# Kernel optimization log

Measured on AMD Instinct MI355X. Metric: run time of the kernel, lower is better.

## Reference

```python
import jax, jax.numpy as jnp
import numpy as np

N, C, S = 16, 512, 4096

def setup_inputs() -> dict:
    rng = jax.random.key(0)
    k1, k2, k3 = jax.random.split(rng, 3)
    return {
        "key": jax.random.normal(k1, (N, C, S), dtype=jnp.float32),
        "value": jax.random.normal(k2, (N, C, S), dtype=jnp.float32),
        "query": jax.random.normal(k3, (N, C, S), dtype=jnp.float32),
    }

def reference(key, value, query):
    KC = key.shape[1]
    # query.permute(0,2,1): [N, C, S] -> [N, S, C]
    # sim_map = bmm(key, query^T): [N, C, C], scaled by KC^-0.5
    sim = jnp.einsum("ncs,nds->ncd", key, query) * (KC ** -0.5)
    # softmax over dim=1 (first C axis)
    sim = jax.nn.softmax(sim, axis=1)
    # context = bmm(sim, value): [N, C, C] @ [N, C, S] -> [N, C, S]
    context = jnp.einsum("ncd,nds->ncs", sim, value)
    return context
```

## Files before the change

### kernel.cpp

```cpp
#include <hip/hip_runtime.h>

typedef __bf16 bf16x8 __attribute__((ext_vector_type(8)));
typedef float f32x4 __attribute__((ext_vector_type(4)));
typedef unsigned short u16;
typedef u16 u16x4 __attribute__((ext_vector_type(4)));
typedef u16 u16x8 __attribute__((ext_vector_type(8)));

__device__ __forceinline__ u16 f2bf(float f) {
  unsigned u = __builtin_bit_cast(unsigned, f);
  unsigned r = (u + 0x7fffu + ((u >> 16) & 1u)) >> 16;
  return (u16)r;
}

__device__ __forceinline__ void gld_lds16(const u16* g, u16* l) {
  __builtin_amdgcn_global_load_lds(
      (__attribute__((address_space(1))) void*)(g),
      (__attribute__((address_space(3))) void*)(l), 16, 0, 0);
}

__device__ __forceinline__ f32x4 ntload4(const float* p) {
  return __builtin_nontemporal_load((const f32x4*)p);
}

__global__ __launch_bounds__(256) void k_cvt(const float* __restrict__ K,
                                             const float* __restrict__ Q,
                                             u16* __restrict__ Kb,
                                             u16* __restrict__ Qb) {
  const float* src = blockIdx.y ? Q : K;
  u16* dst = blockIdx.y ? Qb : Kb;
  const size_t base = (size_t)blockIdx.x * 4096;
  const int t = threadIdx.x;
  f32x4 v[4];
#pragma unroll
  for (int c = 0; c < 4; ++c)
    v[c] = ntload4(src + base + c * 1024 + t * 4);
#pragma unroll
  for (int c = 0; c < 4; ++c) {
    u16x4 h;
    h[0] = f2bf(v[c][0]); h[1] = f2bf(v[c][1]); h[2] = f2bf(v[c][2]); h[3] = f2bf(v[c][3]);
    *(u16x4*)(dst + base + c * 1024 + t * 4) = h;
  }
}

template <int KDIV>
__global__ __launch_bounds__(512) void k_simk(const u16* __restrict__ Kb,
                                              const u16* __restrict__ Qb,
                                              float* __restrict__ Lp) {
  __shared__ u16 sA[2][128 * 64];
  __shared__ u16 sB[2][128 * 64];
  constexpr int NB = 256 * KDIV;
  const int bid = blockIdx.x;
  const int sid = (bid & 7) * (NB / 8) + (bid >> 3);
  constexpr int PER_N = 16 * KDIV;
  const int n = sid / PER_N;
  const int rem = sid % PER_N;
  const int kc = rem >> 4;
  const int r2 = rem & 15;
  const int cy = r2 >> 2, dx = r2 & 3;
  const int t = threadIdx.x, lane = t & 63, wid = t >> 6;
  const int wr = wid >> 2, wc = wid & 3;
  const float scale = 0.04419417382415922f;

  const u16* Ab = Kb + ((size_t)n * 512 + cy * 128) * 4096 + kc * (4096 / KDIV);
  const u16* Bb = Qb + ((size_t)n * 512 + dx * 128) * 4096 + kc * (4096 / KDIV);
  f32x4 acc[4][2] = {};
  const int srow0 = t >> 3;
  const int scol = ((t & 7) << 3) ^ ((srow0 & 7) << 3);

#define SIM_STAGE(buf, k0)                                                      \
  {                                                                             \
    _Pragma("unroll") for (int q = 0; q < 2; ++q) {                             \
      const int row = q * 64 + srow0;                                           \
      gld_lds16(Ab + (size_t)row * 4096 + (k0) + scol,                          \
                &sA[buf][(q * 512 + (wid << 6)) * 8]);                          \
      gld_lds16(Bb + (size_t)row * 4096 + (k0) + scol,                          \
                &sB[buf][(q * 512 + (wid << 6)) * 8]);                          \
    }                                                                           \
  }
#define SIM_COMPUTE(buf)                                                        \
  {                                                                             \
    _Pragma("unroll") for (int ki = 0; ki < 2; ++ki) {                          \
      bf16x8 a[4], b[2];                                                        \
      const int ce = ki * 32 + (lane >> 4) * 8;                                 \
      _Pragma("unroll") for (int mi = 0; mi < 4; ++mi) {                        \
        const int r = wr * 64 + mi * 16 + (lane & 15);                          \
        a[mi] = *(const bf16x8*)&sA[buf][r * 64 + (ce ^ ((r & 7) << 3))];       \
      }                                                                         \
      _Pragma("unroll") for (int ni = 0; ni < 2; ++ni) {                        \
        const int r = wc * 32 + ni * 16 + (lane & 15);                          \
        b[ni] = *(const bf16x8*)&sB[buf][r * 64 + (ce ^ ((r & 7) << 3))];       \
      }                                                                         \
      _Pragma("unroll") for (int mi = 0; mi < 4; ++mi)                          \
        _Pragma("unroll") for (int ni = 0; ni < 2; ++ni)                        \
          acc[mi][ni] = __builtin_amdgcn_mfma_f32_16x16x32_bf16(                \
              a[mi], b[ni], acc[mi][ni], 0, 0, 0);                              \
    }                                                                           \
  }

  constexpr int NSTEP = 64 / KDIV;
  SIM_STAGE(0, 0);
  __syncthreads();
  int cur = 0;
  for (int kt = 0; kt < NSTEP - 1; ++kt) {
    SIM_STAGE(cur ^ 1, (kt + 1) << 6);
    SIM_COMPUTE(cur);
    __syncthreads();
    cur ^= 1;
  }
  SIM_COMPUTE(cur);

  float* Lb = Lp + ((size_t)kc * 16 + n) * 512 * 512;
  const int c0 = cy * 128, d0 = dx * 128;
#pragma unroll
  for (int mi = 0; mi < 4; ++mi)
#pragma unroll
    for (int ni = 0; ni < 2; ++ni) {
      int colo = d0 + wc * 32 + ni * 16 + (lane & 15);
#pragma unroll
      for (int j = 0; j < 4; ++j) {
        int rowo = c0 + wr * 64 + mi * 16 + ((lane >> 4) << 2) + j;
        Lb[(size_t)rowo * 512 + colo] = acc[mi][ni][j] * scale;
      }
    }
#undef SIM_STAGE
#undef SIM_COMPUTE
}

__global__ __launch_bounds__(512) void k_mix(const u16* __restrict__ Kb,
                                             const u16* __restrict__ Qb,
                                             float* __restrict__ Lp,
                                             const float* __restrict__ V,
                                             u16* __restrict__ Vt) {
  extern __shared__ char raw[];
  const int bid = blockIdx.x;
  const int t = threadIdx.x;

  if (bid % 5 == 0) {
    u16* sA = (u16*)raw;
    u16* sB = (u16*)(raw + 32768);
    const int sid0 = bid / 5;
    const int sid = (sid0 & 7) * 64 + (sid0 >> 3);
    const int n = sid >> 5;
    const int rem = sid & 31;
    const int kc = rem >> 4;
    const int r2 = rem & 15;
    const int cy = r2 >> 2, dx = r2 & 3;
    const int lane = t & 63, wid = t >> 6;
    const int wr = wid >> 2, wc = wid & 3;
    const float scale = 0.04419417382415922f;

    const u16* Ab = Kb + ((size_t)n * 512 + cy * 128) * 4096 + kc * 2048;
    const u16* Bb = Qb + ((size_t)n * 512 + dx * 128) * 4096 + kc * 2048;
    f32x4 acc[4][2] = {};
    const int srow0 = t >> 3;
    const int scol = ((t & 7) << 3) ^ ((srow0 & 7) << 3);

#define MIX_STAGE(buf, k0)                                                      \
  {                                                                             \
    _Pragma("unroll") for (int q = 0; q < 2; ++q) {                             \
      const int row = q * 64 + srow0;                                           \
      gld_lds16(Ab + (size_t)row * 4096 + (k0) + scol,                          \
                sA + (buf) * 8192 + (q * 512 + (wid << 6)) * 8);                \
      gld_lds16(Bb + (size_t)row * 4096 + (k0) + scol,                          \
                sB + (buf) * 8192 + (q * 512 + (wid << 6)) * 8);                \
    }                                                                           \
  }
#define MIX_COMPUTE(buf)                                                        \
  {                                                                             \
    _Pragma("unroll") for (int ki = 0; ki < 2; ++ki) {                          \
      bf16x8 a[4], b[2];                                                        \
      const int ce = ki * 32 + (lane >> 4) * 8;                                 \
      _Pragma("unroll") for (int mi = 0; mi < 4; ++mi) {                        \
        const int r = wr * 64 + mi * 16 + (lane & 15);                          \
        a[mi] = *(const bf16x8*)&sA[(buf) * 8192 + r * 64 + (ce ^ ((r & 7) << 3))]; \
      }                                                                         \
      _Pragma("unroll") for (int ni = 0; ni < 2; ++ni) {                        \
        const int r = wc * 32 + ni * 16 + (lane & 15);                          \
        b[ni] = *(const bf16x8*)&sB[(buf) * 8192 + r * 64 + (ce ^ ((r & 7) << 3))]; \
      }                                                                         \
      _Pragma("unroll") for (int mi = 0; mi < 4; ++mi)                          \
        _Pragma("unroll") for (int ni = 0; ni < 2; ++ni)                        \
          acc[mi][ni] = __builtin_amdgcn_mfma_f32_16x16x32_bf16(                \
              a[mi], b[ni], acc[mi][ni], 0, 0, 0);                              \
    }                                                                           \
  }

    MIX_STAGE(0, 0);
    __syncthreads();
    int cur = 0;
    for (int kt = 0; kt < 31; ++kt) {
      MIX_STAGE(cur ^ 1, (kt + 1) << 6);
      MIX_COMPUTE(cur);
      __syncthreads();
      cur ^= 1;
    }
    MIX_COMPUTE(cur);

    float* Lb = Lp + ((size_t)kc * 16 + n) * 512 * 512;
    const int c0 = cy * 128, d0 = dx * 128;
#pragma unroll
    for (int mi = 0; mi < 4; ++mi)
#pragma unroll
      for (int ni = 0; ni < 2; ++ni) {
        int colo = d0 + wc * 32 + ni * 16 + (lane & 15);
#pragma unroll
        for (int j = 0; j < 4; ++j) {
          int rowo = c0 + wr * 64 + mi * 16 + ((lane >> 4) << 2) + j;
          Lb[(size_t)rowo * 512 + colo] = acc[mi][ni][j] * scale;
        }
      }
#undef MIX_STAGE
#undef MIX_COMPUTE
  } else {
    const int vid = bid - bid / 5 - 1;
    const int sub = t >> 8, tt = t & 255;
    const int tile = vid * 2 + sub;
    const int n = tile >> 8;
    const int r = tile & 255;
    const int d0 = (r >> 6) * 128, s0 = (r & 63) * 64;
    float* lds = (float*)(raw + sub * 34816);
    {
      const int r0 = tt >> 4, c4 = (tt & 15) << 2;
#pragma unroll
      for (int p = 0; p < 8; ++p) {
        const int dr = r0 + p * 16;
        f32x4 v = ntload4(V + ((size_t)n * 512 + d0 + dr) * 4096 + s0 + c4);
        const int sw = ((dr >> 3) & 7) << 2;
        *(f32x4*)(&lds[dr * 68 + (c4 ^ sw)]) = v;
      }
    }
    __syncthreads();
    {
      const int sr0 = tt >> 4, dcol = (tt & 15) << 3;
#pragma unroll
      for (int p2 = 0; p2 < 4; ++p2) {
        const int sr = sr0 + p2 * 16;
        u16x8 h;
#pragma unroll
        for (int j = 0; j < 8; ++j) {
          const int d = dcol + j;
          h[j] = f2bf(lds[d * 68 + (sr ^ (((d >> 3) & 7) << 2))]);
        }
        *(u16x8*)(Vt + ((size_t)n * 4096 + s0 + sr) * 512 + d0 + dcol) = h;
      }
    }
  }
}

template <int KDIV>
__global__ __launch_bounds__(256) void k_stats(const float* __restrict__ Lp,
                                               u16* __restrict__ E) {
  __shared__ float redm[8][32];
  __shared__ float reds[8][32];
  const int n = blockIdx.y;
  const int d0 = blockIdx.x * 32;
  const int tx = threadIdx.x & 31, ty = threadIdx.x >> 5;
  const size_t CH = (size_t)16 * 512 * 512;
  const float* B = Lp + (size_t)n * 512 * 512 + d0 + tx;

  float m = -3.0e38f, s = 0.f;
  for (int c = ty; c < 512; c += 8) {
    float v = B[(size_t)c * 512];
#pragma unroll
    for (int q = 1; q < KDIV; ++q) v += B[q * CH + (size_t)c * 512];
    float nm = fmaxf(m, v);
    s = s * __expf(m - nm) + __expf(v - nm);
    m = nm;
  }
  redm[ty][tx] = m;
  reds[ty][tx] = s;
  __syncthreads();
  float M = redm[0][tx];
#pragma unroll
  for (int q = 1; q < 8; ++q) M = fmaxf(M, redm[q][tx]);
  float S = 0.f;
#pragma unroll
  for (int q = 0; q < 8; ++q) S += reds[q][tx] * __expf(redm[q][tx] - M);
  const float si = 1.0f / S;

  u16* Eb = E + (size_t)n * 512 * 512 + d0 + tx;
  for (int c = ty; c < 512; c += 8) {
    float v = B[(size_t)c * 512];
#pragma unroll
    for (int q = 1; q < KDIV; ++q) v += B[q * CH + (size_t)c * 512];
    Eb[(size_t)c * 512] = f2bf(__expf(v - M) * si);
  }
}

__global__ __launch_bounds__(256) void k_vt(const float* __restrict__ V,
                                            u16* __restrict__ Vt) {
  __shared__ float lds[128 * 68];
  const int n = blockIdx.z, d0 = blockIdx.y * 128, s0 = blockIdx.x * 64;
  const int t = threadIdx.x;
  {
    const int r0 = t >> 4, c4 = (t & 15) << 2;
#pragma unroll
    for (int p = 0; p < 8; ++p) {
      const int dr = r0 + p * 16;
      f32x4 v = ntload4(V + ((size_t)n * 512 + d0 + dr) * 4096 + s0 + c4);
      const int sw = ((dr >> 3) & 7) << 2;
      *(f32x4*)(&lds[dr * 68 + (c4 ^ sw)]) = v;
    }
  }
  __syncthreads();
  {
    const int sr0 = t >> 4, dcol = (t & 15) << 3;
#pragma unroll
    for (int p2 = 0; p2 < 4; ++p2) {
      const int sr = sr0 + p2 * 16;
      u16x8 h;
#pragma unroll
      for (int j = 0; j < 8; ++j) {
        const int d = dcol + j;
        h[j] = f2bf(lds[d * 68 + (sr ^ (((d >> 3) & 7) << 2))]);
      }
      *(u16x8*)(Vt + ((size_t)n * 4096 + s0 + sr) * 512 + d0 + dcol) = h;
    }
  }
}

__global__ __launch_bounds__(256) void k_ctx2(const u16* __restrict__ E,
                                              const u16* __restrict__ Vt,
                                              float* __restrict__ O) {
  __shared__ u16 sA[128 * 64];
  __shared__ u16 sB[128 * 64];
  const int bid = blockIdx.x;
  const int sid = (bid & 7) * 256 + (bid >> 3);
  const int n = sid >> 7;
  const int rem = sid & 127;
  const int cy = rem >> 5, sx = rem & 31;
  const int t = threadIdx.x, lane = t & 63, wid = t >> 6;
  const int wr = wid >> 1, wc = wid & 1;

  const u16* Ab = E + ((size_t)n * 512 + cy * 128) * 512;
  const u16* Bb = Vt + ((size_t)n * 4096 + sx * 128) * 512;
  const int srow0 = t >> 3;
  const int scol = ((t & 7) << 3) ^ ((srow0 & 7) << 3);
  f32x4 acc[4][4] = {};

  for (int kd = 0; kd < 512; kd += 64) {
#pragma unroll
    for (int p = 0; p < 4; ++p) {
      const int row = srow0 + p * 32;
      gld_lds16(Ab + (size_t)row * 512 + kd + scol, &sA[(p * 256 + (wid << 6)) * 8]);
      gld_lds16(Bb + (size_t)row * 512 + kd + scol, &sB[(p * 256 + (wid << 6)) * 8]);
    }
    __syncthreads();
#pragma unroll
    for (int ki = 0; ki < 2; ++ki) {
      bf16x8 a[4], b[4];
      const int ce = ki * 32 + (lane >> 4) * 8;
#pragma unroll
      for (int mi = 0; mi < 4; ++mi) {
        const int r = wr * 64 + mi * 16 + (lane & 15);
        a[mi] = *(const bf16x8*)&sA[r * 64 + (ce ^ ((r & 7) << 3))];
      }
#pragma unroll
      for (int ni = 0; ni < 4; ++ni) {
        const int r = wc * 64 + ni * 16 + (lane & 15);
        b[ni] = *(const bf16x8*)&sB[r * 64 + (ce ^ ((r & 7) << 3))];
      }
#pragma unroll
      for (int mi = 0; mi < 4; ++mi)
#pragma unroll
        for (int ni = 0; ni < 4; ++ni)
          acc[mi][ni] = __builtin_amdgcn_mfma_f32_16x16x32_bf16(a[mi], b[ni], acc[mi][ni], 0, 0, 0);
    }
    __syncthreads();
  }
  float* Ob = O + ((size_t)n * 512 + cy * 128) * 4096 + sx * 128;
#pragma unroll
  for (int mi = 0; mi < 4; ++mi)
#pragma unroll
    for (int ni = 0; ni < 4; ++ni) {
      int colo = wc * 64 + ni * 16 + (lane & 15);
#pragma unroll
      for (int j = 0; j < 4; ++j) {
        int rowo = wr * 64 + mi * 16 + ((lane >> 4) << 2) + j;
        __builtin_nontemporal_store(acc[mi][ni][j], &Ob[(size_t)rowo * 4096 + colo]);
      }
    }
}

extern "C" void kernel_launch(void* const* d_in, const int* in_sizes, int n_in,
                              void* d_out, int out_size, void* d_ws, size_t ws_size,
                              hipStream_t stream) {
  const float* Kp = (const float*)d_in[0];
  const float* Vp = (const float*)d_in[1];
  const float* Qp = (const float*)d_in[2];
  float* Op = (float*)d_out;
  char* ws = (char*)d_ws;
  const size_t MB = 1024 * 1024;

  if (ws_size >= 192 * MB) {
    u16* Kb = (u16*)ws;
    u16* Qb = (u16*)(ws + 64 * MB);
    u16* Vt = (u16*)(ws + 128 * MB);
    u16* E  = (u16*)(ws + 64 * MB);
    float* Lp = Op;

    k_cvt<<<dim3(8192, 2), 256, 0, stream>>>(Kp, Qp, Kb, Qb);
    k_mix<<<2560, 512, 69632, stream>>>(Kb, Qb, Lp, Vp, Vt);
    k_stats<2><<<dim3(16, 16), 256, 0, stream>>>(Lp, E);
    k_ctx2<<<2048, 256, 0, stream>>>(E, Vt, Op);
  } else if (ws_size >= 128 * MB) {
    u16* Kb = (u16*)ws;
    u16* Qb = (u16*)(ws + 64 * MB);
    u16* Vt = (u16*)ws;
    u16* E  = (u16*)(ws + 64 * MB);
    float* Lp = Op;

    k_cvt<<<dim3(8192, 2), 256, 0, stream>>>(Kp, Qp, Kb, Qb);
    k_simk<2><<<512, 512, 0, stream>>>(Kb, Qb, Lp);
    k_stats<2><<<dim3(16, 16), 256, 0, stream>>>(Lp, E);
    k_vt<<<dim3(64, 4, 16), 256, 0, stream>>>(Vp, Vt);
    k_ctx2<<<2048, 256, 0, stream>>>(E, Vt, Op);
  }
}
```

Measured before the change: 241.8 us.

## Fuse K/Q bf16 conversion into similarity GEMM by loading fp32 tiles directly

```diff
diff --git a/kernel.cpp b/kernel.cpp
--- a/kernel.cpp
+++ b/kernel.cpp
@@ -12,6 +12,18 @@
   return (u16)r;
 }
 
+__device__ __forceinline__ bf16x8 cvt8v(f32x4 a, f32x4 b) {
+  bf16x8 h;
+  h[0] = (__bf16)a[0]; h[1] = (__bf16)a[1]; h[2] = (__bf16)a[2]; h[3] = (__bf16)a[3];
+  h[4] = (__bf16)b[0]; h[5] = (__bf16)b[1]; h[6] = (__bf16)b[2]; h[7] = (__bf16)b[3];
+  return h;
+}
+
+__device__ __forceinline__ void gld_lds16f(const float* g, float* l) {
+  __builtin_amdgcn_global_load_lds(
+      (__attribute__((address_space(1))) void*)(g),
+      (__attribute__((address_space(3))) void*)(l), 16, 0, 0);
+}
 __device__ __forceinline__ void gld_lds16(const u16* g, u16* l) {
   __builtin_amdgcn_global_load_lds(
       (__attribute__((address_space(1))) void*)(g),
@@ -20,6 +32,205 @@
 
 __device__ __forceinline__ f32x4 ntload4(const float* p) {
   return __builtin_nontemporal_load((const f32x4*)p);
+}
+
+__global__ __launch_bounds__(512) void k_mixf(const float* __restrict__ K,
+                                              const float* __restrict__ Q,
+                                              float* __restrict__ Lp,
+                                              const float* __restrict__ V,
+                                              u16* __restrict__ Vt) {
+  extern __shared__ char raw[];
+  const int bid = blockIdx.x;
+  const int t = threadIdx.x;
+
+  if (bid % 5 == 0) {
+    float* sAf = (float*)raw;
+    float* sBf = (float*)(raw + 32768);
+    const int sid0 = bid / 5;
+    const int sid = (sid0 & 7) * 64 + (sid0 >> 3);
+    const int n = sid >> 5;
+    const int rem = sid & 31;
+    const int kc = rem >> 4;
+    const int r2 = rem & 15;
+    const int cy = r2 >> 2, dx = r2 & 3;
+    const int lane = t & 63, wid = t >> 6;
+    const int wr = wid >> 2, wc = wid & 3;
+    const float scale = 0.04419417382415922f;
+
+    const float* Ab = K + ((size_t)n * 512 + cy * 128) * 4096 + kc * 2048;
+    const float* Bb = Q + ((size_t)n * 512 + dx * 128) * 4096 + kc * 2048;
+    f32x4 acc[4][2] = {};
+
+    const int srow0 = t >> 3;
+    const int scol = ((t & 7) << 2) ^ ((srow0 & 7) << 2);
+
+#define MF_STAGE(buf, k0)                                                       \
+  {                                                                             \
+    _Pragma("unroll") for (int q = 0; q < 2; ++q) {                             \
+      const int row = q * 64 + srow0;                                           \
+      gld_lds16f(Ab + (size_t)row * 4096 + (k0) + scol,                         \
+                 sAf + (buf) * 4096 + (q * 512 + (wid << 6)) * 4);              \
+      gld_lds16f(Bb + (size_t)row * 4096 + (k0) + scol,                         \
+                 sBf + (buf) * 4096 + (q * 512 + (wid << 6)) * 4);              \
+    }                                                                           \
+  }
+#define MF_COMPUTE(buf)                                                         \
+  {                                                                             \
+    bf16x8 a[4], b[2];                                                          \
+    const int cb = (lane >> 4) << 3;                                            \
+    _Pragma("unroll") for (int mi = 0; mi < 4; ++mi) {                          \
+      const int r = wr * 64 + mi * 16 + (lane & 15);                            \
+      const int sz = (r & 7) << 2;                                              \
+      const float* p = sAf + (buf) * 4096 + r * 32;                             \
+      a[mi] = cvt8v(*(const f32x4*)(p + (cb ^ sz)),                             \
+                    *(const f32x4*)(p + ((cb + 4) ^ sz)));                      \
+    }                                                                           \
+    _Pragma("unroll") for (int ni = 0; ni < 2; ++ni) {                          \
+      const int r = wc * 32 + ni * 16 + (lane & 15);                            \
+      const int sz = (r & 7) << 2;                                              \
+      const float* p = sBf + (buf) * 4096 + r * 32;                             \
+      b[ni] = cvt8v(*(const f32x4*)(p + (cb ^ sz)),                             \
+                    *(const f32x4*)(p + ((cb + 4) ^ sz)));                      \
+    }                                                                           \
+    _Pragma("unroll") for (int mi = 0; mi < 4; ++mi)                            \
+      _Pragma("unroll") for (int ni = 0; ni < 2; ++ni)                          \
+        acc[mi][ni] = __builtin_amdgcn_mfma_f32_16x16x32_bf16(                  \
+            a[mi], b[ni], acc[mi][ni], 0, 0, 0);                                \
+  }
+
+    MF_STAGE(0, 0);
+    __syncthreads();
+    int cur = 0;
+#pragma unroll 1
+    for (int kt = 0; kt < 63; ++kt) {
+      MF_STAGE(cur ^ 1, (kt + 1) * 32);
+      MF_COMPUTE(cur);
+      __syncthreads();
+      cur ^= 1;
+    }
+    MF_COMPUTE(cur);
+
+    float* Lb = Lp + ((size_t)kc * 16 + n) * 512 * 512;
+    const int c0 = cy * 128, d0 = dx * 128;
+#pragma unroll
+    for (int mi = 0; mi < 4; ++mi)
+#pragma unroll
+      for (int ni = 0; ni < 2; ++ni) {
+        int colo = d0 + wc * 32 + ni * 16 + (lane & 15);
+#pragma unroll
+        for (int j = 0; j < 4; ++j) {
+          int rowo = c0 + wr * 64 + mi * 16 + ((lane >> 4) << 2) + j;
+          Lb[(size_t)rowo * 512 + colo] = acc[mi][ni][j] * scale;
+        }
+      }
+#undef MF_STAGE
+#undef MF_COMPUTE
+  } else {
+    const int vid = bid - bid / 5 - 1;
+    const int sub = t >> 8, tt = t & 255;
+    const int tile = vid * 2 + sub;
+    const int n = tile >> 8;
+    const int r = tile & 255;
+    const int d0 = (r >> 6) * 128, s0 = (r & 63) * 64;
+    float* lds = (float*)(raw + sub * 34816);
+    {
+      const int r0 = tt >> 4, c4 = (tt & 15) << 2;
+#pragma unroll
+      for (int p = 0; p < 8; ++p) {
+        const int dr = r0 + p * 16;
+        f32x4 v = ntload4(V + ((size_t)n * 512 + d0 + dr) * 4096 + s0 + c4);
+        const int sw = ((dr >> 3) & 7) << 2;
+        *(f32x4*)(&lds[dr * 68 + (c4 ^ sw)]) = v;
+      }
+    }
+    __syncthreads();
+    {
+      const int sr0 = tt >> 4, dcol = (tt & 15) << 3;
+#pragma unroll
+      for (int p2 = 0; p2 < 4; ++p2) {
+        const int sr = sr0 + p2 * 16;
+        u16x8 h;
+#pragma unroll
+        for (int j = 0; j < 8; ++j) {
+          const int d = dcol + j;
+          h[j] = f2bf(lds[d * 68 + (sr ^ (((d >> 3) & 7) << 2))]);
+        }
+        *(u16x8*)(Vt + ((size_t)n * 4096 + s0 + sr) * 512 + d0 + dcol) = h;
+      }
+    }
+  }
+}
+
+template <int KDIV>
+__global__ __launch_bounds__(256) void k_stats(const float* __restrict__ Lp,
+                                               u16* __restrict__ E) {
+  __shared__ float redm[8][32];
+  __shared__ float reds[8][32];
+  const int n = blockIdx.y;
+  const int d0 = blockIdx.x * 32;
+  const int tx = threadIdx.x & 31, ty = threadIdx.x >> 5;
+  const size_t CH = (size_t)16 * 512 * 512;
+  const float* B = Lp + (size_t)n * 512 * 512 + d0 + tx;
+
+  float m = -3.0e38f, s = 0.f;
+  for (int c = ty; c < 512; c += 8) {
+    float v = B[(size_t)c * 512];
+#pragma unroll
+    for (int q = 1; q < KDIV; ++q) v += B[q * CH + (size_t)c * 512];
+    float nm = fmaxf(m, v);
+    s = s * __expf(m - nm) + __expf(v - nm);
+    m = nm;
+  }
+  redm[ty][tx] = m;
+  reds[ty][tx] = s;
+  __syncthreads();
+  float M = redm[0][tx];
+#pragma unroll
+  for (int q = 1; q < 8; ++q) M = fmaxf(M, redm[q][tx]);
+  float S = 0.f;
+#pragma unroll
+  for (int q = 0; q < 8; ++q) S += reds[q][tx] * __expf(redm[q][tx] - M);
+  const float si = 1.0f / S;
+
+  u16* Eb = E + (size_t)n * 512 * 512 + d0 + tx;
+  for (int c = ty; c < 512; c += 8) {
+    float v = B[(size_t)c * 512];
+#pragma unroll
+    for (int q = 1; q < KDIV; ++q) v += B[q * CH + (size_t)c * 512];
+    Eb[(size_t)c * 512] = f2bf(__expf(v - M) * si);
+  }
+}
+
+__global__ __launch_bounds__(256) void k_vt(const float* __restrict__ V,
+                                            u16* __restrict__ Vt) {
+  __shared__ float lds[128 * 68];
+  const int n = blockIdx.z, d0 = blockIdx.y * 128, s0 = blockIdx.x * 64;
+  const int t = threadIdx.x;
+  {
+    const int r0 = t >> 4, c4 = (t & 15) << 2;
+#pragma unroll
+    for (int p = 0; p < 8; ++p) {
+      const int dr = r0 + p * 16;
+      f32x4 v = ntload4(V + ((size_t)n * 512 + d0 + dr) * 4096 + s0 + c4);
+      const int sw = ((dr >> 3) & 7) << 2;
+      *(f32x4*)(&lds[dr * 68 + (c4 ^ sw)]) = v;
+    }
+  }
+  __syncthreads();
+  {
+    const int sr0 = t >> 4, dcol = (t & 15) << 3;
+#pragma unroll
+    for (int p2 = 0; p2 < 4; ++p2) {
+      const int sr = sr0 + p2 * 16;
+      u16x8 h;
+#pragma unroll
+      for (int j = 0; j < 8; ++j) {
+        const int d = dcol + j;
+        h[j] = f2bf(lds[d * 68 + (sr ^ (((d >> 3) & 7) << 2))]);
+      }
+      *(u16x8*)(Vt + ((size_t)n * 4096 + s0 + sr) * 512 + d0 + dcol) = h;
+    }
+  }
 }
 
 __global__ __launch_bounds__(256) void k_cvt(const float* __restrict__ K,
@@ -126,199 +337,6 @@
 #undef SIM_COMPUTE
 }
 
-__global__ __launch_bounds__(512) void k_mix(const u16* __restrict__ Kb,
-                                             const u16* __restrict__ Qb,
-                                             float* __restrict__ Lp,
-                                             const float* __restrict__ V,
-                                             u16* __restrict__ Vt) {
-  extern __shared__ char raw[];
-  const int bid = blockIdx.x;
-  const int t = threadIdx.x;
-
-  if (bid % 5 == 0) {
-    u16* sA = (u16*)raw;
-    u16* sB = (u16*)(raw + 32768);
-    const int sid0 = bid / 5;
-    const int sid = (sid0 & 7) * 64 + (sid0 >> 3);
-    const int n = sid >> 5;
-    const int rem = sid & 31;
-    const int kc = rem >> 4;
-    const int r2 = rem & 15;
-    const int cy = r2 >> 2, dx = r2 & 3;
-    const int lane = t & 63, wid = t >> 6;
-    const int wr = wid >> 2, wc = wid & 3;
-    const float scale = 0.04419417382415922f;
-
-    const u16* Ab = Kb + ((size_t)n * 512 + cy * 128) * 4096 + kc * 2048;
-    const u16* Bb = Qb + ((size_t)n * 512 + dx * 128) * 4096 + kc * 2048;
-    f32x4 acc[4][2] = {};
-    const int srow0 = t >> 3;
-    const int scol = ((t & 7) << 3) ^ ((srow0 & 7) << 3);
-
-#define MIX_STAGE(buf, k0)                                                      \
-  {                                                                             \
-    _Pragma("unroll") for (int q = 0; q < 2; ++q) {                             \
-      const int row = q * 64 + srow0;                                           \
-      gld_lds16(Ab + (size_t)row * 4096 + (k0) + scol,                          \
-                sA + (buf) * 8192 + (q * 512 + (wid << 6)) * 8);                \
-      gld_lds16(Bb + (size_t)row * 4096 + (k0) + scol,                          \
-                sB + (buf) * 8192 + (q * 512 + (wid << 6)) * 8);                \
-    }                                                                           \
-  }
-#define MIX_COMPUTE(buf)                                                        \
-  {                                                                             \
-    _Pragma("unroll") for (int ki = 0; ki < 2; ++ki) {                          \
-      bf16x8 a[4], b[2];                                                        \
-      const int ce = ki * 32 + (lane >> 4) * 8;                                 \
-      _Pragma("unroll") for (int mi = 0; mi < 4; ++mi) {                        \
-        const int r = wr * 64 + mi * 16 + (lane & 15);                          \
-        a[mi] = *(const bf16x8*)&sA[(buf) * 8192 + r * 64 + (ce ^ ((r & 7) << 3))]; \
-      }                                                                         \
-      _Pragma("unroll") for (int ni = 0; ni < 2; ++ni) {                        \
-        const int r = wc * 32 + ni * 16 + (lane & 15);                          \
-        b[ni] = *(const bf16x8*)&sB[(buf) * 8192 + r * 64 + (ce ^ ((r & 7) << 3))]; \
-      }                                                                         \
-      _Pragma("unroll") for (int mi = 0; mi < 4; ++mi)                          \
-        _Pragma("unroll") for (int ni = 0; ni < 2; ++ni)                        \
-          acc[mi][ni] = __builtin_amdgcn_mfma_f32_16x16x32_bf16(                \
-              a[mi], b[ni], acc[mi][ni], 0, 0, 0);                              \
-    }                                                                           \
-  }
-
-    MIX_STAGE(0, 0);
-    __syncthreads();
-    int cur = 0;
-    for (int kt = 0; kt < 31; ++kt) {
-      MIX_STAGE(cur ^ 1, (kt + 1) << 6);
-      MIX_COMPUTE(cur);
-      __syncthreads();
-      cur ^= 1;
-    }
-    MIX_COMPUTE(cur);
-
-    float* Lb = Lp + ((size_t)kc * 16 + n) * 512 * 512;
-    const int c0 = cy * 128, d0 = dx * 128;
-#pragma unroll
-    for (int mi = 0; mi < 4; ++mi)
-#pragma unroll
-      for (int ni = 0; ni < 2; ++ni) {
-        int colo = d0 + wc * 32 + ni * 16 + (lane & 15);
-#pragma unroll
-        for (int j = 0; j < 4; ++j) {
-          int rowo = c0 + wr * 64 + mi * 16 + ((lane >> 4) << 2) + j;
-          Lb[(size_t)rowo * 512 + colo] = acc[mi][ni][j] * scale;
-        }
-      }
-#undef MIX_STAGE
-#undef MIX_COMPUTE
-  } else {
-    const int vid = bid - bid / 5 - 1;
-    const int sub = t >> 8, tt = t & 255;
-    const int tile = vid * 2 + sub;
-    const int n = tile >> 8;
-    const int r = tile & 255;
-    const int d0 = (r >> 6) * 128, s0 = (r & 63) * 64;
-    float* lds = (float*)(raw + sub * 34816);
-    {
-      const int r0 = tt >> 4, c4 = (tt & 15) << 2;
-#pragma unroll
-      for (int p = 0; p < 8; ++p) {
-        const int dr = r0 + p * 16;
-        f32x4 v = ntload4(V + ((size_t)n * 512 + d0 + dr) * 4096 + s0 + c4);
-        const int sw = ((dr >> 3) & 7) << 2;
-        *(f32x4*)(&lds[dr * 68 + (c4 ^ sw)]) = v;
-      }
-    }
-    __syncthreads();
-    {
-      const int sr0 = tt >> 4, dcol = (tt & 15) << 3;
-#pragma unroll
-      for (int p2 = 0; p2 < 4; ++p2) {
-        const int sr = sr0 + p2 * 16;
-        u16x8 h;
-#pragma unroll
-        for (int j = 0; j < 8; ++j) {
-          const int d = dcol + j;
-          h[j] = f2bf(lds[d * 68 + (sr ^ (((d >> 3) & 7) << 2))]);
-        }
-        *(u16x8*)(Vt + ((size_t)n * 4096 + s0 + sr) * 512 + d0 + dcol) = h;
-      }
-    }
-  }
-}
-
-template <int KDIV>
-__global__ __launch_bounds__(256) void k_stats(const float* __restrict__ Lp,
-                                               u16* __restrict__ E) {
-  __shared__ float redm[8][32];
-  __shared__ float reds[8][32];
-  const int n = blockIdx.y;
-  const int d0 = blockIdx.x * 32;
-  const int tx = threadIdx.x & 31, ty = threadIdx.x >> 5;
-  const size_t CH = (size_t)16 * 512 * 512;
-  const float* B = Lp + (size_t)n * 512 * 512 + d0 + tx;
-
-  float m = -3.0e38f, s = 0.f;
-  for (int c = ty; c < 512; c += 8) {
-    float v = B[(size_t)c * 512];
-#pragma unroll
-    for (int q = 1; q < KDIV; ++q) v += B[q * CH + (size_t)c * 512];
-    float nm = fmaxf(m, v);
-    s = s * __expf(m - nm) + __expf(v - nm);
-    m = nm;
-  }
-  redm[ty][tx] = m;
-  reds[ty][tx] = s;
-  __syncthreads();
-  float M = redm[0][tx];
-#pragma unroll
-  for (int q = 1; q < 8; ++q) M = fmaxf(M, redm[q][tx]);
-  float S = 0.f;
-#pragma unroll
-  for (int q = 0; q < 8; ++q) S += reds[q][tx] * __expf(redm[q][tx] - M);
-  const float si = 1.0f / S;
-
-  u16* Eb = E + (size_t)n * 512 * 512 + d0 + tx;
-  for (int c = ty; c < 512; c += 8) {
-    float v = B[(size_t)c * 512];
-#pragma unroll
-    for (int q = 1; q < KDIV; ++q) v += B[q * CH + (size_t)c * 512];
-    Eb[(size_t)c * 512] = f2bf(__expf(v - M) * si);
-  }
-}
-
-__global__ __launch_bounds__(256) void k_vt(const float* __restrict__ V,
-                                            u16* __restrict__ Vt) {
-  __shared__ float lds[128 * 68];
-  const int n = blockIdx.z, d0 = blockIdx.y * 128, s0 = blockIdx.x * 64;
-  const int t = threadIdx.x;
-  {
-    const int r0 = t >> 4, c4 = (t & 15) << 2;
-#pragma unroll
-    for (int p = 0; p < 8; ++p) {
-      const int dr = r0 + p * 16;
-      f32x4 v = ntload4(V + ((size_t)n * 512 + d0 + dr) * 4096 + s0 + c4);
-      const int sw = ((dr >> 3) & 7) << 2;
-      *(f32x4*)(&lds[dr * 68 + (c4 ^ sw)]) = v;
-    }
-  }
-  __syncthreads();
-  {
-    const int sr0 = t >> 4, dcol = (t & 15) << 3;
-#pragma unroll
-    for (int p2 = 0; p2 < 4; ++p2) {
-      const int sr = sr0 + p2 * 16;
-      u16x8 h;
-#pragma unroll
-      for (int j = 0; j < 8; ++j) {
-        const int d = dcol + j;
-        h[j] = f2bf(lds[d * 68 + (sr ^ (((d >> 3) & 7) << 2))]);
-      }
-      *(u16x8*)(Vt + ((size_t)n * 4096 + s0 + sr) * 512 + d0 + dcol) = h;
-    }
-  }
-}
-
 __global__ __launch_bounds__(256) void k_ctx2(const u16* __restrict__ E,
                                               const u16* __restrict__ Vt,
                                               float* __restrict__ O) {
@@ -392,28 +410,21 @@
   char* ws = (char*)d_ws;
   const size_t MB = 1024 * 1024;
 
-  if (ws_size >= 192 * MB) {
-    u16* Kb = (u16*)ws;
-    u16* Qb = (u16*)(ws + 64 * MB);
-    u16* Vt = (u16*)(ws + 128 * MB);
-    u16* E  = (u16*)(ws + 64 * MB);
-    float* Lp = Op;
-
-    k_cvt<<<dim3(8192, 2), 256, 0, stream>>>(Kp, Qp, Kb, Qb);
-    k_mix<<<2560, 512, 69632, stream>>>(Kb, Qb, Lp, Vp, Vt);
-    k_stats<2><<<dim3(16, 16), 256, 0, stream>>>(Lp, E);
-    k_ctx2<<<2048, 256, 0, stream>>>(E, Vt, Op);
-  } else if (ws_size >= 128 * MB) {
-    u16* Kb = (u16*)ws;
-    u16* Qb = (u16*)(ws + 64 * MB);
+  if (ws_size >= 128 * MB) {
     u16* Vt = (u16*)ws;
     u16* E  = (u16*)(ws + 64 * MB);
     float* Lp = Op;
 
-    k_cvt<<<dim3(8192, 2), 256, 0, stream>>>(Kp, Qp, Kb, Qb);
-    k_simk<2><<<512, 512, 0, stream>>>(Kb, Qb, Lp);
+    k_mixf<<<2560, 512, 69632, stream>>>(Kp, Qp, Lp, Vp, Vt);
     k_stats<2><<<dim3(16, 16), 256, 0, stream>>>(Lp, E);
-    k_vt<<<dim3(64, 4, 16), 256, 0, stream>>>(Vp, Vt);
     k_ctx2<<<2048, 256, 0, stream>>>(E, Vt, Op);
-  }
-}
+  } else if (ws_size >= 72 * MB) {
+    u16* Vt = (u16*)ws;
+    u16* E  = (u16*)(ws + 64 * MB);
+    float* Lp = Op;
+
+    k_mixf<<<2560, 512, 69632, stream>>>(Kp, Qp, Lp, Vp, Vt);
+    k_stats<2><<<dim3(16, 16), 256, 0, stream>>>(Lp, E);
+    k_ctx2<<<2048, 256, 0, stream>>>(E, Vt, Op);
+  }
+}
```

Result: slower. 257.2 us (+6.3%).

## Double-buffer context GEMM with 8 waves and raise MFMA priority in sim

Applied to the files above, without the earlier changes.

```diff
diff --git a/kernel.cpp b/kernel.cpp
--- a/kernel.cpp
+++ b/kernel.cpp
@@ -39,6 +39,169 @@
     u16x4 h;
     h[0] = f2bf(v[c][0]); h[1] = f2bf(v[c][1]); h[2] = f2bf(v[c][2]); h[3] = f2bf(v[c][3]);
     *(u16x4*)(dst + base + c * 1024 + t * 4) = h;
+  }
+}
+
+__global__ __launch_bounds__(512) void k_mix(const u16* __restrict__ Kb,
+                                             const u16* __restrict__ Qb,
+                                             float* __restrict__ Lp,
+                                             const float* __restrict__ V,
+                                             u16* __restrict__ Vt) {
+  extern __shared__ char raw[];
+  const int bid = blockIdx.x;
+  const int t = threadIdx.x;
+
+  if (bid % 5 == 0) {
+    u16* sA = (u16*)raw;
+    u16* sB = (u16*)(raw + 32768);
+    const int sid0 = bid / 5;
+    const int sid = (sid0 & 7) * 64 + (sid0 >> 3);
+    const int n = sid >> 5;
+    const int rem = sid & 31;
+    const int kc = rem >> 4;
+    const int r2 = rem & 15;
+    const int cy = r2 >> 2, dx = r2 & 3;
+    const int lane = t & 63, wid = t >> 6;
+    const int wr = wid >> 2, wc = wid & 3;
+    const float scale = 0.04419417382415922f;
+
+    const u16* Ab = Kb + ((size_t)n * 512 + cy * 128) * 4096 + kc * 2048;
+    const u16* Bb = Qb + ((size_t)n * 512 + dx * 128) * 4096 + kc * 2048;
+    f32x4 acc[4][2] = {};
+    const int srow0 = t >> 3;
+    const int scol = ((t & 7) << 3) ^ ((srow0 & 7) << 3);
+
+#define MIX_STAGE(buf, k0)                                                      \
+  {                                                                             \
+    _Pragma("unroll") for (int q = 0; q < 2; ++q) {                             \
+      const int row = q * 64 + srow0;                                           \
+      gld_lds16(Ab + (size_t)row * 4096 + (k0) + scol,                          \
+                sA + (buf) * 8192 + (q * 512 + (wid << 6)) * 8);                \
+      gld_lds16(Bb + (size_t)row * 4096 + (k0) + scol,                          \
+                sB + (buf) * 8192 + (q * 512 + (wid << 6)) * 8);                \
+    }                                                                           \
+  }
+#define MIX_COMPUTE(buf)                                                        \
+  {                                                                             \
+    _Pragma("unroll") for (int ki = 0; ki < 2; ++ki) {                          \
+      bf16x8 a[4], b[2];                                                        \
+      const int ce = ki * 32 + (lane >> 4) * 8;                                 \
+      _Pragma("unroll") for (int mi = 0; mi < 4; ++mi) {                        \
+        const int r = wr * 64 + mi * 16 + (lane & 15);                          \
+        a[mi] = *(const bf16x8*)&sA[(buf) * 8192 + r * 64 + (ce ^ ((r & 7) << 3))]; \
+      }                                                                         \
+      _Pragma("unroll") for (int ni = 0; ni < 2; ++ni) {                        \
+        const int r = wc * 32 + ni * 16 + (lane & 15);                          \
+        b[ni] = *(const bf16x8*)&sB[(buf) * 8192 + r * 64 + (ce ^ ((r & 7) << 3))]; \
+      }                                                                         \
+      __builtin_amdgcn_s_setprio(1);                                            \
+      _Pragma("unroll") for (int mi = 0; mi < 4; ++mi)                          \
+        _Pragma("unroll") for (int ni = 0; ni < 2; ++ni)                        \
+          acc[mi][ni] = __builtin_amdgcn_mfma_f32_16x16x32_bf16(                \
+              a[mi], b[ni], acc[mi][ni], 0, 0, 0);                              \
+      __builtin_amdgcn_s_setprio(0);                                            \
+    }                                                                           \
+  }
+
+    MIX_STAGE(0, 0);
+    __syncthreads();
+    int cur = 0;
+    for (int kt = 0; kt < 31; ++kt) {
+      MIX_STAGE(cur ^ 1, (kt + 1) << 6);
+      MIX_COMPUTE(cur);
+      __syncthreads();
+      cur ^= 1;
+    }
+    MIX_COMPUTE(cur);
+
+    float* Lb = Lp + ((size_t)kc * 16 + n) * 512 * 512;
+    const int c0 = cy * 128, d0 = dx * 128;
+#pragma unroll
+    for (int mi = 0; mi < 4; ++mi)
+#pragma unroll
+      for (int ni = 0; ni < 2; ++ni) {
+        int colo = d0 + wc * 32 + ni * 16 + (lane & 15);
+#pragma unroll
+        for (int j = 0; j < 4; ++j) {
+          int rowo = c0 + wr * 64 + mi * 16 + ((lane >> 4) << 2) + j;
+          Lb[(size_t)rowo * 512 + colo] = acc[mi][ni][j] * scale;
+        }
+      }
+#undef MIX_STAGE
+#undef MIX_COMPUTE
+  } else {
+    const int vid = bid - bid / 5 - 1;
+    const int sub = t >> 8, tt = t & 255;
+    const int tile = vid * 2 + sub;
+    const int n = tile >> 8;
+    const int r = tile & 255;
+    const int d0 = (r >> 6) * 128, s0 = (r & 63) * 64;
+    float* lds = (float*)(raw + sub * 34816);
+    {
+      const int r0 = tt >> 4, c4 = (tt & 15) << 2;
+#pragma unroll
+      for (int p = 0; p < 8; ++p) {
+        const int dr = r0 + p * 16;
+        f32x4 v = ntload4(V + ((size_t)n * 512 + d0 + dr) * 4096 + s0 + c4);
+        const int sw = ((dr >> 3) & 7) << 2;
+        *(f32x4*)(&lds[dr * 68 + (c4 ^ sw)]) = v;
+      }
+    }
+    __syncthreads();
+    {
+      const int sr0 = tt >> 4, dcol = (tt & 15) << 3;
+#pragma unroll
+      for (int p2 = 0; p2 < 4; ++p2) {
+        const int sr = sr0 + p2 * 16;
+        u16x8 h;
+#pragma unroll
+        for (int j = 0; j < 8; ++j) {
+          const int d = dcol + j;
+          h[j] = f2bf(lds[d * 68 + (sr ^ (((d >> 3) & 7) << 2))]);
+        }
+        *(u16x8*)(Vt + ((size_t)n * 4096 + s0 + sr) * 512 + d0 + dcol) = h;
+      }
+    }
+  }
+}
+
+template <int KDIV>
+__global__ __launch_bounds__(256) void k_stats(const float* __restrict__ Lp,
+                                               u16* __restrict__ E) {
+  __shared__ float redm[8][32];
+  __shared__ float reds[8][32];
+  const int n = blockIdx.y;
+  const int d0 = blockIdx.x * 32;
+  const int tx = threadIdx.x & 31, ty = threadIdx.x >> 5;
+  const size_t CH = (size_t)16 * 512 * 512;
+  const float* B = Lp + (size_t)n * 512 * 512 + d0 + tx;
+
+  float m = -3.0e38f, s = 0.f;
+  for (int c = ty; c < 512; c += 8) {
+    float v = B[(size_t)c * 512];
+#pragma unroll
+    for (int q = 1; q < KDIV; ++q) v += B[q * CH + (size_t)c * 512];
+    float nm = fmaxf(m, v);
+    s = s * __expf(m - nm) + __expf(v - nm);
+    m = nm;
+  }
+  redm[ty][tx] = m;
+  reds[ty][tx] = s;
+  __syncthreads();
+  float M = redm[0][tx];
+#pragma unroll
+  for (int q = 1; q < 8; ++q) M = fmaxf(M, redm[q][tx]);
+  float S = 0.f;
+#pragma unroll
+  for (int q = 0; q < 8; ++q) S += reds[q][tx] * __expf(redm[q][tx] - M);
+  const float si = 1.0f / S;
+
+  u16* Eb = E + (size_t)n * 512 * 512 + d0 + tx;
+  for (int c = ty; c < 512; c += 8) {
+    float v = B[(size_t)c * 512];
+#pragma unroll
+    for (int q = 1; q < KDIV; ++q) v += B[q * CH + (size_t)c * 512];
+    Eb[(size_t)c * 512] = f2bf(__expf(v - M) * si);
   }
 }
 
@@ -126,167 +289,6 @@
 #undef SIM_COMPUTE
 }
 
-__global__ __launch_bounds__(512) void k_mix(const u16* __restrict__ Kb,
-                                             const u16* __restrict__ Qb,
-                                             float* __restrict__ Lp,
-                                             const float* __restrict__ V,
-                                             u16* __restrict__ Vt) {
-  extern __shared__ char raw[];
-  const int bid = blockIdx.x;
-  const int t = threadIdx.x;
-
-  if (bid % 5 == 0) {
-    u16* sA = (u16*)raw;
-    u16* sB = (u16*)(raw + 32768);
-    const int sid0 = bid / 5;
-    const int sid = (sid0 & 7) * 64 + (sid0 >> 3);
-    const int n = sid >> 5;
-    const int rem = sid & 31;
-    const int kc = rem >> 4;
-    const int r2 = rem & 15;
-    const int cy = r2 >> 2, dx = r2 & 3;
-    const int lane = t & 63, wid = t >> 6;
-    const int wr = wid >> 2, wc = wid & 3;
-    const float scale = 0.04419417382415922f;
-
-    const u16* Ab = Kb + ((size_t)n * 512 + cy * 128) * 4096 + kc * 2048;
-    const u16* Bb = Qb + ((size_t)n * 512 + dx * 128) * 4096 + kc * 2048;
-    f32x4 acc[4][2] = {};
-    const int srow0 = t >> 3;
-    const int scol = ((t & 7) << 3) ^ ((srow0 & 7) << 3);
-
-#define MIX_STAGE(buf, k0)                                                      \
-  {                                                                             \
-    _Pragma("unroll") for (int q = 0; q < 2; ++q) {                             \
-      const int row = q * 64 + srow0;                                           \
-      gld_lds16(Ab + (size_t)row * 4096 + (k0) + scol,                          \
-                sA + (buf) * 8192 + (q * 512 + (wid << 6)) * 8);                \
-      gld_lds16(Bb + (size_t)row * 4096 + (k0) + scol,                          \
-                sB + (buf) * 8192 + (q * 512 + (wid << 6)) * 8);                \
-    }                                                                           \
-  }
-#define MIX_COMPUTE(buf)                                                        \
-  {                                                                             \
-    _Pragma("unroll") for (int ki = 0; ki < 2; ++ki) {                          \
-      bf16x8 a[4], b[2];                                                        \
-      const int ce = ki * 32 + (lane >> 4) * 8;                                 \
-      _Pragma("unroll") for (int mi = 0; mi < 4; ++mi) {                        \
-        const int r = wr * 64 + mi * 16 + (lane & 15);                          \
-        a[mi] = *(const bf16x8*)&sA[(buf) * 8192 + r * 64 + (ce ^ ((r & 7) << 3))]; \
-      }                                                                         \
-      _Pragma("unroll") for (int ni = 0; ni < 2; ++ni) {                        \
-        const int r = wc * 32 + ni * 16 + (lane & 15);                          \
-        b[ni] = *(const bf16x8*)&sB[(buf) * 8192 + r * 64 + (ce ^ ((r & 7) << 3))]; \
-      }                                                                         \
-      _Pragma("unroll") for (int mi = 0; mi < 4; ++mi)                          \
-        _Pragma("unroll") for (int ni = 0; ni < 2; ++ni)                        \
-          acc[mi][ni] = __builtin_amdgcn_mfma_f32_16x16x32_bf16(                \
-              a[mi], b[ni], acc[mi][ni], 0, 0, 0);                              \
-    }                                                                           \
-  }
-
-    MIX_STAGE(0, 0);
-    __syncthreads();
-    int cur = 0;
-    for (int kt = 0; kt < 31; ++kt) {
-      MIX_STAGE(cur ^ 1, (kt + 1) << 6);
-      MIX_COMPUTE(cur);
-      __syncthreads();
-      cur ^= 1;
-    }
-    MIX_COMPUTE(cur);
-
-    float* Lb = Lp + ((size_t)kc * 16 + n) * 512 * 512;
-    const int c0 = cy * 128, d0 = dx * 128;
-#pragma unroll
-    for (int mi = 0; mi < 4; ++mi)
-#pragma unroll
-      for (int ni = 0; ni < 2; ++ni) {
-        int colo = d0 + wc * 32 + ni * 16 + (lane & 15);
-#pragma unroll
-        for (int j = 0; j < 4; ++j) {
-          int rowo = c0 + wr * 64 + mi * 16 + ((lane >> 4) << 2) + j;
-          Lb[(size_t)rowo * 512 + colo] = acc[mi][ni][j] * scale;
-        }
-      }
-#undef MIX_STAGE
-#undef MIX_COMPUTE
-  } else {
-    const int vid = bid - bid / 5 - 1;
-    const int sub = t >> 8, tt = t & 255;
-    const int tile = vid * 2 + sub;
-    const int n = tile >> 8;
-    const int r = tile & 255;
-    const int d0 = (r >> 6) * 128, s0 = (r & 63) * 64;
-    float* lds = (float*)(raw + sub * 34816);
-    {
-      const int r0 = tt >> 4, c4 = (tt & 15) << 2;
-#pragma unroll
-      for (int p = 0; p < 8; ++p) {
-        const int dr = r0 + p * 16;
-        f32x4 v = ntload4(V + ((size_t)n * 512 + d0 + dr) * 4096 + s0 + c4);
-        const int sw = ((dr >> 3) & 7) << 2;
-        *(f32x4*)(&lds[dr * 68 + (c4 ^ sw)]) = v;
-      }
-    }
-    __syncthreads();
-    {
-      const int sr0 = tt >> 4, dcol = (tt & 15) << 3;
-#pragma unroll
-      for (int p2 = 0; p2 < 4; ++p2) {
-        const int sr = sr0 + p2 * 16;
-        u16x8 h;
-#pragma unroll
-        for (int j = 0; j < 8; ++j) {
-          const int d = dcol + j;
-          h[j] = f2bf(lds[d * 68 + (sr ^ (((d >> 3) & 7) << 2))]);
-        }
-        *(u16x8*)(Vt + ((size_t)n * 4096 + s0 + sr) * 512 + d0 + dcol) = h;
-      }
-    }
-  }
-}
-
-template <int KDIV>
-__global__ __launch_bounds__(256) void k_stats(const float* __restrict__ Lp,
-                                               u16* __restrict__ E) {
-  __shared__ float redm[8][32];
-  __shared__ float reds[8][32];
-  const int n = blockIdx.y;
-  const int d0 = blockIdx.x * 32;
-  const int tx = threadIdx.x & 31, ty = threadIdx.x >> 5;
-  const size_t CH = (size_t)16 * 512 * 512;
-  const float* B = Lp + (size_t)n * 512 * 512 + d0 + tx;
-
-  float m = -3.0e38f, s = 0.f;
-  for (int c = ty; c < 512; c += 8) {
-    float v = B[(size_t)c * 512];
-#pragma unroll
-    for (int q = 1; q < KDIV; ++q) v += B[q * CH + (size_t)c * 512];
-    float nm = fmaxf(m, v);
-    s = s * __expf(m - nm) + __expf(v - nm);
-    m = nm;
-  }
-  redm[ty][tx] = m;
-  reds[ty][tx] = s;
-  __syncthreads();
-  float M = redm[0][tx];
-#pragma unroll
-  for (int q = 1; q < 8; ++q) M = fmaxf(M, redm[q][tx]);
-  float S = 0.f;
-#pragma unroll
-  for (int q = 0; q < 8; ++q) S += reds[q][tx] * __expf(redm[q][tx] - M);
-  const float si = 1.0f / S;
-
-  u16* Eb = E + (size_t)n * 512 * 512 + d0 + tx;
-  for (int c = ty; c < 512; c += 8) {
-    float v = B[(size_t)c * 512];
-#pragma unroll
-    for (int q = 1; q < KDIV; ++q) v += B[q * CH + (size_t)c * 512];
-    Eb[(size_t)c * 512] = f2bf(__expf(v - M) * si);
-  }
-}
-
 __global__ __launch_bounds__(256) void k_vt(const float* __restrict__ V,
                                             u16* __restrict__ Vt) {
   __shared__ float lds[128 * 68];
@@ -319,67 +321,80 @@
   }
 }
 
-__global__ __launch_bounds__(256) void k_ctx2(const u16* __restrict__ E,
+__global__ __launch_bounds__(512) void k_ctx3(const u16* __restrict__ E,
                                               const u16* __restrict__ Vt,
                                               float* __restrict__ O) {
-  __shared__ u16 sA[128 * 64];
-  __shared__ u16 sB[128 * 64];
+  __shared__ u16 sA[2][128 * 64];
+  __shared__ u16 sB[2][128 * 64];
   const int bid = blockIdx.x;
   const int sid = (bid & 7) * 256 + (bid >> 3);
   const int n = sid >> 7;
   const int rem = sid & 127;
   const int cy = rem >> 5, sx = rem & 31;
   const int t = threadIdx.x, lane = t & 63, wid = t >> 6;
-  const int wr = wid >> 1, wc = wid & 1;
+  const int wr = wid >> 2, wc = wid & 3;
 
   const u16* Ab = E + ((size_t)n * 512 + cy * 128) * 512;
   const u16* Bb = Vt + ((size_t)n * 4096 + sx * 128) * 512;
   const int srow0 = t >> 3;
   const int scol = ((t & 7) << 3) ^ ((srow0 & 7) << 3);
-  f32x4 acc[4][4] = {};
-
-  for (int kd = 0; kd < 512; kd += 64) {
-#pragma unroll
-    for (int p = 0; p < 4; ++p) {
-      const int row = srow0 + p * 32;
-      gld_lds16(Ab + (size_t)row * 512 + kd + scol, &sA[(p * 256 + (wid << 6)) * 8]);
-      gld_lds16(Bb + (size_t)row * 512 + kd + scol, &sB[(p * 256 + (wid << 6)) * 8]);
-    }
+  f32x4 acc[4][2] = {};
+
+#define CTX_STAGE(buf, kd)                                                      \
+  {                                                                             \
+    _Pragma("unroll") for (int q = 0; q < 2; ++q) {                             \
+      const int row = q * 64 + srow0;                                           \
+      gld_lds16(Ab + (size_t)row * 512 + (kd) + scol,                           \
+                &sA[buf][(q * 512 + (wid << 6)) * 8]);                          \
+      gld_lds16(Bb + (size_t)row * 512 + (kd) + scol,                           \
+                &sB[buf][(q * 512 + (wid << 6)) * 8]);                          \
+    }                                                                           \
+  }
+#define CTX_COMPUTE(buf)                                                        \
+  {                                                                             \
+    _Pragma("unroll") for (int ki = 0; ki < 2; ++ki) {                          \
+      bf16x8 a[4], b[2];                                                        \
+      const int ce = ki * 32 + (lane >> 4) * 8;                                 \
+      _Pragma("unroll") for (int mi = 0; mi < 4; ++mi) {                        \
+        const int r = wr * 64 + mi * 16 + (lane & 15);                          \
+        a[mi] = *(const bf16x8*)&sA[buf][r * 64 + (ce ^ ((r & 7) << 3))];       \
+      }                                                                         \
+      _Pragma("unroll") for (int ni = 0; ni < 2; ++ni) {                        \
+        const int r = wc * 32 + ni * 16 + (lane & 15);                          \
+        b[ni] = *(const bf16x8*)&sB[buf][r * 64 + (ce ^ ((r & 7) << 3))];       \
+      }                                                                         \
+      _Pragma("unroll") for (int mi = 0; mi < 4; ++mi)                          \
+        _Pragma("unroll") for (int ni = 0; ni < 2; ++ni)                        \
+          acc[mi][ni] = __builtin_amdgcn_mfma_f32_16x16x32_bf16(                \
+              a[mi], b[ni], acc[mi][ni], 0, 0, 0);                              \
+    }                                                                           \
+  }
+
+  CTX_STAGE(0, 0);
+  __syncthreads();
+  int cur = 0;
+  for (int kt = 0; kt < 7; ++kt) {
+    CTX_STAGE(cur ^ 1, (kt + 1) << 6);
+    CTX_COMPUTE(cur);
     __syncthreads();
-#pragma unroll
-    for (int ki = 0; ki < 2; ++ki) {
-      bf16x8 a[4], b[4];
-      const int ce = ki * 32 + (lane >> 4) * 8;
-#pragma unroll
-      for (int mi = 0; mi < 4; ++mi) {
-        const int r = wr * 64 + mi * 16 + (lane & 15);
-        a[mi] = *(const bf16x8*)&sA[r * 64 + (ce ^ ((r & 7) << 3))];
-      }
-#pragma unroll
-      for (int ni = 0; ni < 4; ++ni) {
-        const int r = wc * 64 + ni * 16 + (lane & 15);
-        b[ni] = *(const bf16x8*)&sB[r * 64 + (ce ^ ((r & 7) << 3))];
-      }
-#pragma unroll
-      for (int mi = 0; mi < 4; ++mi)
-#pragma unroll
-        for (int ni = 0; ni < 4; ++ni)
-          acc[mi][ni] = __builtin_amdgcn_mfma_f32_16x16x32_bf16(a[mi], b[ni], acc[mi][ni], 0, 0, 0);
-    }
-    __syncthreads();
-  }
+    cur ^= 1;
+  }
+  CTX_COMPUTE(cur);
+
   float* Ob = O + ((size_t)n * 512 + cy * 128) * 4096 + sx * 128;
 #pragma unroll
   for (int mi = 0; mi < 4; ++mi)
 #pragma unroll
-    for (int ni = 0; ni < 4; ++ni) {
-      int colo = wc * 64 + ni * 16 + (lane & 15);
+    for (int ni = 0; ni < 2; ++ni) {
+      int colo = wc * 32 + ni * 16 + (lane & 15);
 #pragma unroll
       for (int j = 0; j < 4; ++j) {
         int rowo = wr * 64 + mi * 16 + ((lane >> 4) << 2) + j;
         __builtin_nontemporal_store(acc[mi][ni][j], &Ob[(size_t)rowo * 4096 + colo]);
       }
     }
+#undef CTX_STAGE
+#undef CTX_COMPUTE
 }
 
 extern "C" void kernel_launch(void* const* d_in, const int* in_sizes, int n_in,
@@ -402,7 +417,7 @@
     k_cvt<<<dim3(8192, 2), 256, 0, stream>>>(Kp, Qp, Kb, Qb);
     k_mix<<<2560, 512, 69632, stream>>>(Kb, Qb, Lp, Vp, Vt);
     k_stats<2><<<dim3(16, 16), 256, 0, stream>>>(Lp, E);
-    k_ctx2<<<2048, 256, 0, stream>>>(E, Vt, Op);
+    k_ctx3<<<2048, 512, 0, stream>>>(E, Vt, Op);
   } else if (ws_size >= 128 * MB) {
     u16* Kb = (u16*)ws;
     u16* Qb = (u16*)(ws + 64 * MB);
@@ -414,6 +429,6 @@
     k_simk<2><<<512, 512, 0, stream>>>(Kb, Qb, Lp);
     k_stats<2><<<dim3(16, 16), 256, 0, stream>>>(Lp, E);
     k_vt<<<dim3(64, 4, 16), 256, 0, stream>>>(Vp, Vt);
-    k_ctx2<<<2048, 256, 0, stream>>>(E, Vt, Op);
-  }
-}
+    k_ctx3<<<2048, 512, 0, stream>>>(E, Vt, Op);
+  }
+}
```

Measured after the change: 239.5 us. Within noise of the previous version (-1.0%).
